# Optimization experiments

Measured on AMD Instinct MI355X. Metric: run time of the kernel, lower is better.

The kernel has to match this reference:

```python
import jax, jax.numpy as jnp
import numpy as np

B, N, HID, NHEADS, VOCAB = 8, 2048, 768, 4, 15
ALPHA = 0.2  # LeakyReLU negative slope
NEG = -9e15  # matches -9000000000000000.0 mask constant


def setup_inputs() -> dict:
    key = jax.random.key(0)
    ks = jax.random.split(key, 7)
    node_feats = jax.random.randint(ks[0], (B, N), 0, VOCAB, dtype=jnp.int32)
    adjs = jax.random.randint(ks[1], (B, N, N), 0, 2, dtype=jnp.int32)
    embed_table = jax.random.normal(ks[2], (VOCAB, HID), dtype=jnp.float32)
    W_heads = jax.random.normal(ks[3], (NHEADS, HID, HID), dtype=jnp.float32) * 0.05
    a_heads = jax.random.normal(ks[4], (NHEADS, 2 * HID, 1), dtype=jnp.float32) * 0.05
    W_out = jax.random.normal(ks[5], (NHEADS * HID, HID), dtype=jnp.float32) * 0.05
    a_out = jax.random.normal(ks[6], (2 * HID, 1), dtype=jnp.float32) * 0.05
    return {"node_feats": node_feats, "adjs": adjs, "embed_table": embed_table,
            "W_heads": W_heads, "a_heads": a_heads, "W_out": W_out, "a_out": a_out}


def gat_layer(h, adj, W, a, concat):
    # h: (B,N,Fin), adj: (B,N,N), W: (Fin,Fout), a: (2*Fout,1)
    Fout = W.shape[1]
    Wh = jnp.matmul(h, W)                      # (B,N,Fout)
    Wh1 = jnp.matmul(Wh, a[:Fout])             # (B,N,1)
    Wh2 = jnp.matmul(Wh, a[Fout:])             # (B,N,1)
    e = Wh1 + jnp.swapaxes(Wh2, 1, 2)          # (B,N,N)
    e = jax.nn.leaky_relu(e, negative_slope=ALPHA)
    e = jnp.where(adj > 0, e, NEG)
    att = jax.nn.softmax(e, axis=-1)           # (B,N,N)
    h_prime = jnp.matmul(att, Wh)              # (B,N,Fout)
    return jax.nn.elu(h_prime) if concat else h_prime


def reference(node_feats, adjs, embed_table, W_heads, a_heads, W_out, a_out):
    x = embed_table[node_feats]                # (B,N,HID)  (shape_enc treated as identity)
    # multi-head GAT, heads vmapped then concatenated along feature dim
    heads = jax.vmap(lambda W, a: gat_layer(x, adjs, W, a, concat=True))(W_heads, a_heads)
    x = jnp.concatenate(jnp.moveaxis(heads, 0, -2).reshape(B, N, 1, NHEADS * HID).squeeze(2)[None], axis=0)[0] if False else jnp.transpose(heads, (1, 2, 0, 3)).reshape(B, N, NHEADS * HID)
    x = jax.nn.elu(gat_layer(x, adjs, W_out, a_out, concat=False))  # (B,N,HID)
    # pooling_forward with all-ones mask -> masked mean over node dim
    sum_emb = jnp.sum(x, axis=1)               # (B,HID)
    denom = jnp.maximum(jnp.full_like(sum_emb, float(N)), 1e-9)
    return sum_emb / denom                     # (B,HID)
```

## Files before the change

kernel.cpp:

```cpp
#include <hip/hip_runtime.h>
#include <math.h>

#define BB 8
#define NN 2048
#define HID 768
#define NHEADS 4
#define VOCAB 15
#define ALPHA 0.2f
#define NEGV -9e15f
#define MTOT (BB * NN)

using short4v = __attribute__((ext_vector_type(4))) short;
using short8v = __attribute__((ext_vector_type(8))) short;
using f32x4 = __attribute__((ext_vector_type(4))) float;

__device__ __forceinline__ short f2bf(float f) {
  union { float f; unsigned u; } x;
  x.f = f;
  unsigned r = x.u + 0x7fffu + ((x.u >> 16) & 1u);
  return (short)(r >> 16);
}

__device__ __forceinline__ void cp16(const void* g, void* l) {
  __builtin_amdgcn_global_load_lds(
      (const __attribute__((address_space(1))) unsigned int*)g,
      (__attribute__((address_space(3))) unsigned int*)l, 16, 0, 0);
}

__device__ __forceinline__ unsigned long long nibcompress(unsigned long long x) {
  x = (x | (x >> 4)) & 0x00FF00FF00FF00FFull;
  x = (x | (x >> 8)) & 0x0000FFFF0000FFFFull;
  x = (x | (x >> 16)) & 0x00000000FFFFFFFFull;
  return x;
}

#define MEMFENCE asm volatile("" ::: "memory")
#define SBAR()                         \
  do {                                 \
    MEMFENCE;                          \
    __builtin_amdgcn_s_barrier();      \
    MEMFENCE;                          \
  } while (0)

#define PACK_B 32768
#define ZERO_B 308
#define NFM_B 64
#define TRAN_B 2304
#define TW_B 192
__global__ __launch_bounds__(256) void setup_kernel(
    const int* __restrict__ adj, unsigned long long* __restrict__ packed,
    float* __restrict__ zbase, const int* __restrict__ nf,
    unsigned long long* __restrict__ nfm, const float* __restrict__ W_out,
    short* __restrict__ Wt_o, const float* __restrict__ table,
    const float* __restrict__ W_heads, float* __restrict__ TWp) {
  const int bid = blockIdx.x;
  const int tid = threadIdx.x;
  if (bid < PACK_B) {
    __shared__ unsigned long long nibq[32];
    long base = (long)bid * 1024;
    int4 a = *(const int4*)(adj + base + tid * 4);
    unsigned nib = (a.x > 0 ? 1u : 0u) | (a.y > 0 ? 2u : 0u) |
                   (a.z > 0 ? 4u : 0u) | (a.w > 0 ? 8u : 0u);
    ((unsigned char*)nibq)[tid] = (unsigned char)nib;
    __syncthreads();
    if (tid < 16) {
      unsigned long long lo = nibcompress(nibq[2 * tid]);
      unsigned long long hi = nibcompress(nibq[2 * tid + 1]);
      packed[(base >> 6) + tid] = lo | (hi << 32);
    }
  } else if (bid < PACK_B + ZERO_B) {
    zbase[(bid - PACK_B) * 256 + tid] = 0.f;
  } else if (bid < PACK_B + ZERO_B + NFM_B) {
    int r = bid - PACK_B - ZERO_B;
    int b = r >> 3, c = r & 7;
    int w = tid >> 6;
    int j = c * 256 + tid;
    int nfv = nf[b * NN + j];
#pragma unroll
    for (int v = 0; v < VOCAB; ++v) {
      unsigned long long m = __ballot(nfv == v);
      if ((tid & 63) == 0) nfm[((long)b * VOCAB + v) * 32 + c * 4 + w] = m;
    }
  } else if (bid < PACK_B + ZERO_B + NFM_B + TRAN_B) {
    __shared__ float t[32][33];
    int r2 = bid - PACK_B - ZERO_B - NFM_B;
    const int K = NHEADS * HID, N = HID;
    int k0 = (r2 % 96) * 32, n0 = (r2 / 96) * 32;
    int tx = tid & 31, ty = tid >> 5;
#pragma unroll
    for (int i = 0; i < 32; i += 8)
      t[ty + i][tx] = W_out[(long)(k0 + ty + i) * N + n0 + tx];
    __syncthreads();
#pragma unroll
    for (int i = 0; i < 32; i += 8)
      Wt_o[(long)(n0 + ty + i) * K + k0 + tx] = f2bf(t[tx][ty + i]);
  } else {
    __shared__ float tbl[VOCAB][48];
    int r3 = bid - PACK_B - ZERO_B - NFM_B - TRAN_B;
    const int cx = r3 % 12, ky = r3 / 12;
    const int c = cx * 256 + tid;
    const int h = (cx * 256) / HID;
    const int n = c - h * HID;
    const int k0 = ky * 48;
    for (int idx = tid; idx < VOCAB * 48; idx += 256)
      tbl[idx / 48][idx % 48] = table[(idx / 48) * HID + k0 + idx % 48];
    __syncthreads();
    float acc[VOCAB];
#pragma unroll
    for (int v = 0; v < VOCAB; ++v) acc[v] = 0.f;
    const float* wp = W_heads + (long)h * HID * HID + (long)k0 * HID + n;
#pragma unroll 8
    for (int kk = 0; kk < 48; ++kk) {
      float w = wp[(long)kk * HID];
#pragma unroll
      for (int v = 0; v < VOCAB; ++v) acc[v] = fmaf(tbl[v][kk], w, acc[v]);
    }
#pragma unroll
    for (int v = 0; v < VOCAB; ++v)
      TWp[((long)ky * VOCAB + v) * (NHEADS * HID) + c] = acc[v];
  }
}

__global__ __launch_bounds__(256) void tw_finish_kernel(
    const float* __restrict__ TWp, float* __restrict__ TW,
    const float* __restrict__ a_heads, float* __restrict__ TW1,
    float* __restrict__ TW2) {
  const int tid = threadIdx.x;
  const int c = blockIdx.x * 256 + tid;
  const int h = (blockIdx.x * 256) / HID;
  const int n = c - h * HID;
  const float a1 = a_heads[h * 2 * HID + n];
  const float a2 = a_heads[h * 2 * HID + HID + n];
  const int lane = tid & 63;
  const int wv = tid >> 6;
  __shared__ float red[4][2 * VOCAB];

  float s1[VOCAB], s2[VOCAB];
#pragma unroll
  for (int v = 0; v < VOCAB; ++v) {
    float s = 0.f;
#pragma unroll
    for (int ky = 0; ky < 16; ++ky)
      s += TWp[((long)ky * VOCAB + v) * (NHEADS * HID) + c];
    TW[v * (NHEADS * HID) + c] = s;
    s1[v] = s * a1;
    s2[v] = s * a2;
  }
#pragma unroll
  for (int off = 1; off < 64; off <<= 1)
#pragma unroll
    for (int v = 0; v < VOCAB; ++v) {
      s1[v] += __shfl_xor(s1[v], off);
      s2[v] += __shfl_xor(s2[v], off);
    }
  if (lane == 0) {
#pragma unroll
    for (int v = 0; v < VOCAB; ++v) {
      red[wv][v] = s1[v];
      red[wv][VOCAB + v] = s2[v];
    }
  }
  __syncthreads();
  if (tid < 2 * VOCAB) {
    float s = red[0][tid] + red[1][tid] + red[2][tid] + red[3][tid];
    float* dst = (tid < VOCAB) ? (TW1 + h * VOCAB + tid)
                               : (TW2 + h * VOCAB + tid - VOCAB);
    atomicAdd(dst, s);
  }
}

__global__ __launch_bounds__(256) void p16_kernel(
    const int* __restrict__ nf, const unsigned* __restrict__ padj32,
    const unsigned* __restrict__ nfm32, const float* __restrict__ TW1,
    const float* __restrict__ TW2, float* __restrict__ P16) {
  const int t = threadIdx.x;
  const int wv = t >> 6;
  const int lane = t & 63;
  const int rowm = blockIdx.x * 4 + wv;
  const int b = rowm >> 11;
  __shared__ float cnts[4][16];

  unsigned a = padj32[(long)rowm * 64 + lane];
  const unsigned* nb = nfm32 + (long)b * VOCAB * 64 + lane;
  int cnt[VOCAB];
#pragma unroll
  for (int v = 0; v < VOCAB; ++v) cnt[v] = __popc(a & nb[v * 64]);
#pragma unroll
  for (int off = 1; off < 64; off <<= 1)
#pragma unroll
    for (int v = 0; v < VOCAB; ++v) cnt[v] += __shfl_xor(cnt[v], off);
  int cntsum = 0;
#pragma unroll
  for (int v = 0; v < VOCAB; ++v) cntsum += cnt[v];
  const bool use_full = (cntsum == 0);
  if (use_full) {
#pragma unroll
    for (int v = 0; v < VOCAB; ++v) cnt[v] = __popc(nb[v * 64]);
#pragma unroll
    for (int off = 1; off < 64; off <<= 1)
#pragma unroll
      for (int v = 0; v < VOCAB; ++v) cnt[v] += __shfl_xor(cnt[v], off);
  }
  if (lane < 16) cnts[wv][lane] = (lane < VOCAB) ? (float)cnt[lane] : 0.f;
  __syncthreads();

  const int h = lane >> 4;
  const int v = lane & 15;
  const int nfi = nf[b * NN + (rowm & 2047)];
  float cvf = cnts[wv][v];
  bool valid = (v < VOCAB) && (cvf > 0.f);
  float logit = 0.f;
  if (!use_full) {
    float s = TW1[h * VOCAB + nfi] + ((v < VOCAB) ? TW2[h * VOCAB + v] : 0.f);
    logit = s > 0.f ? s : ALPHA * s;
  }
  float mv = valid ? logit : -INFINITY;
#pragma unroll
  for (int off = 1; off < 16; off <<= 1) mv = fmaxf(mv, __shfl_xor(mv, off));
  float pv = valid ? cvf * __expf(logit - mv) : 0.f;
  float sum = pv;
#pragma unroll
  for (int off = 1; off < 16; off <<= 1) sum += __shfl_xor(sum, off);
  if (v < VOCAB) P16[((long)h * 16384 + rowm) * 16 + v] = pv / sum;
}

__global__ __launch_bounds__(256) void hcat_expand(
    const float* __restrict__ TW, const float* __restrict__ P16,
    short* __restrict__ hcat) {
  __shared__ float twl[VOCAB * 128];
  __shared__ float pl[128 * 16];
  const int c0 = blockIdx.x * 128;
  const int r0 = blockIdx.y * 128;
  const int h = c0 / HID;
  const int t = threadIdx.x;
  for (int idx = t; idx < VOCAB * 128; idx += 256)
    twl[idx] = TW[(idx / 128) * (NHEADS * HID) + c0 + (idx & 127)];
  for (int idx = t; idx < 128 * 16; idx += 256)
    pl[idx] = P16[((long)h * 16384 + r0 + (idx >> 4)) * 16 + (idx & 15)];
  __syncthreads();
  const int clb = (t & 31) * 4;
  const int rlb = (t >> 5) * 16;
#pragma unroll 4
  for (int rr = 0; rr < 16; ++rr) {
    int rl = rlb + rr;
    short4v o;
#pragma unroll
    for (int cc = 0; cc < 4; ++cc) {
      float s = 0.f;
#pragma unroll
      for (int vv = 0; vv < VOCAB; ++vv)
        s = fmaf(pl[rl * 16 + vv], twl[vv * 128 + clb + cc], s);
      s = s > 0.f ? s : (__expf(s) - 1.f);
      o[cc] = f2bf(s);
    }
    *(short4v*)(hcat + (long)(r0 + rl) * (NHEADS * HID) + c0 + clb) = o;
  }
}

template <int MODE>
__global__ __launch_bounds__(512, 2) void mfma_gemm(
    const short* __restrict__ A, const short* __restrict__ B,
    int K, int lda, int ldb, long sA, long sB,
    float* __restrict__ Cf, short* __restrict__ Ct,
    const float* __restrict__ a_vec, float* __restrict__ Wh1g,
    float* __restrict__ Wh2g) {
  __shared__ short lds[2][2][16384];

  const int gx = gridDim.x, gy = gridDim.y;
  int linb = blockIdx.x + gx * (blockIdx.y + gy * blockIdx.z);
  const int per = (gx * gy * gridDim.z) >> 3;
  int work = (linb & 7) * per + (linb >> 3);
  const int bx = work % gx;
  int tmpw = work / gx;
  const int by = tmpw % gy;
  const int z = tmpw / gy;

  A += (long)z * sA;
  B += (long)z * sB;

  const int tid = threadIdx.x;
  const int m0 = by * 256;
  const int n0 = bx * 256;
  const int lane = tid & 63;
  const int wid = tid >> 6;
  const int wr = wid >> 2;
  const int wc = wid & 3;
  const int l15 = lane & 15;
  const int quad = lane >> 4;
  const int NT = K >> 6;

  const int cbase = (quad ^ (l15 & 7)) << 3;

  auto stageA = [&](int kt, int h) {
    const short* src = A + (long)(m0 + h * 128) * lda + kt * 64;
    short* dst = &lds[kt & 1][0][h * 8192];
#pragma unroll
    for (int it = 0; it < 2; ++it) {
      int r = it * 64 + (tid >> 3);
      int s = tid & 7;
      cp16(src + (long)r * lda + ((s ^ (r & 7)) << 3),
           dst + (it * 512 + tid) * 8);
    }
  };
  auto stageB = [&](int kt, int h) {
    const short* src = B + (long)(n0 + h * 128) * ldb + kt * 64;
    short* dst = &lds[kt & 1][1][h * 8192];
#pragma unroll
    for (int it = 0; it < 2; ++it) {
      int r = it * 64 + (tid >> 3);
      int s = tid & 7;
      cp16(src + (long)r * ldb + ((s ^ (r & 7)) << 3),
           dst + (it * 512 + tid) * 8);
    }
  };

  f32x4 acc[8][4];
#pragma unroll
  for (int i = 0; i < 8; ++i)
#pragma unroll
    for (int j = 0; j < 4; ++j) acc[i][j] = (f32x4){0.f, 0.f, 0.f, 0.f};

  stageA(0, 0); stageA(0, 1);
  stageB(0, 0); stageB(0, 1);
  stageA(1, 0); stageA(1, 1);
  asm volatile("s_waitcnt vmcnt(4)" ::: "memory");
  SBAR();

#pragma unroll 1
  for (int t = 0; t < NT; ++t) {
    const int p = t & 1;
    const short* Ab = &lds[p][0][0];
    const short* Bb = &lds[p][1][0];
    short8v a[4][2], b0[2][2], b1[2][2];

    if (t + 1 < NT) { stageB(t + 1, 0); stageB(t + 1, 1); }
#pragma unroll
    for (int ii = 0; ii < 4; ++ii) {
      int ro = (wr * 128 + ii * 16 + l15) * 64;
      a[ii][0] = *(const short8v*)(Ab + ro + cbase);
      a[ii][1] = *(const short8v*)(Ab + ro + (cbase ^ 32));
    }
#pragma unroll
    for (int jj = 0; jj < 2; ++jj) {
      int ro = (wc * 64 + jj * 16 + l15) * 64;
      b0[jj][0] = *(const short8v*)(Bb + ro + cbase);
      b0[jj][1] = *(const short8v*)(Bb + ro + (cbase ^ 32));
    }
    SBAR();
    asm volatile("s_waitcnt lgkmcnt(0)" ::: "memory");
    __builtin_amdgcn_sched_barrier(0);
    __builtin_amdgcn_s_setprio(1);
#pragma unroll
    for (int ii = 0; ii < 4; ++ii)
#pragma unroll
      for (int jj = 0; jj < 2; ++jj) {
        acc[ii][jj] = __builtin_amdgcn_mfma_f32_16x16x32_bf16(
            a[ii][0], b0[jj][0], acc[ii][jj], 0, 0, 0);
        acc[ii][jj] = __builtin_amdgcn_mfma_f32_16x16x32_bf16(
            a[ii][1], b0[jj][1], acc[ii][jj], 0, 0, 0);
      }
    __builtin_amdgcn_sched_barrier(0);
    __builtin_amdgcn_s_setprio(0);
    SBAR();

#pragma unroll
    for (int jj = 0; jj < 2; ++jj) {
      int ro = (wc * 64 + 32 + jj * 16 + l15) * 64;
      b1[jj][0] = *(const short8v*)(Bb + ro + cbase);
      b1[jj][1] = *(const short8v*)(Bb + ro + (cbase ^ 32));
    }
    SBAR();
    asm volatile("s_waitcnt lgkmcnt(0)" ::: "memory");
    __builtin_amdgcn_sched_barrier(0);
    __builtin_amdgcn_s_setprio(1);
#pragma unroll
    for (int ii = 0; ii < 4; ++ii)
#pragma unroll
      for (int jj = 0; jj < 2; ++jj) {
        acc[ii][2 + jj] = __builtin_amdgcn_mfma_f32_16x16x32_bf16(
            a[ii][0], b1[jj][0], acc[ii][2 + jj], 0, 0, 0);
        acc[ii][2 + jj] = __builtin_amdgcn_mfma_f32_16x16x32_bf16(
            a[ii][1], b1[jj][1], acc[ii][2 + jj], 0, 0, 0);
      }
    __builtin_amdgcn_sched_barrier(0);
    __builtin_amdgcn_s_setprio(0);
    SBAR();

#pragma unroll
    for (int ii = 0; ii < 4; ++ii) {
      int ro = (wr * 128 + 64 + ii * 16 + l15) * 64;
      a[ii][0] = *(const short8v*)(Ab + ro + cbase);
      a[ii][1] = *(const short8v*)(Ab + ro + (cbase ^ 32));
    }
    SBAR();
    asm volatile("s_waitcnt lgkmcnt(0)" ::: "memory");
    __builtin_amdgcn_sched_barrier(0);
    __builtin_amdgcn_s_setprio(1);
#pragma unroll
    for (int ii = 0; ii < 4; ++ii)
#pragma unroll
      for (int jj = 0; jj < 2; ++jj) {
        acc[4 + ii][2 + jj] = __builtin_amdgcn_mfma_f32_16x16x32_bf16(
            a[ii][0], b1[jj][0], acc[4 + ii][2 + jj], 0, 0, 0);
        acc[4 + ii][2 + jj] = __builtin_amdgcn_mfma_f32_16x16x32_bf16(
            a[ii][1], b1[jj][1], acc[4 + ii][2 + jj], 0, 0, 0);
      }
    __builtin_amdgcn_sched_barrier(0);
    __builtin_amdgcn_s_setprio(0);
    SBAR();

    if (t + 2 < NT) { stageA(t + 2, 0); stageA(t + 2, 1); }
    __builtin_amdgcn_s_setprio(1);
#pragma unroll
    for (int ii = 0; ii < 4; ++ii)
#pragma unroll
      for (int jj = 0; jj < 2; ++jj) {
        acc[4 + ii][jj] = __builtin_amdgcn_mfma_f32_16x16x32_bf16(
            a[ii][0], b0[jj][0], acc[4 + ii][jj], 0, 0, 0);
        acc[4 + ii][jj] = __builtin_amdgcn_mfma_f32_16x16x32_bf16(
            a[ii][1], b0[jj][1], acc[4 + ii][jj], 0, 0, 0);
      }
    __builtin_amdgcn_sched_barrier(0);
    __builtin_amdgcn_s_setprio(0);
    if (t + 2 < NT) {
      asm volatile("s_waitcnt vmcnt(4)" ::: "memory");
    } else if (t + 1 < NT) {
      asm volatile("s_waitcnt vmcnt(0)" ::: "memory");
    }
    SBAR();
  }

  if constexpr (MODE == 3) {
#pragma unroll
    for (int nj = 0; nj < 4; ++nj) {
      int col = n0 + wc * 64 + nj * 16 + l15;
      float s = 0.f;
#pragma unroll
      for (int mi = 0; mi < 8; ++mi)
#pragma unroll
        for (int reg = 0; reg < 4; ++reg) {
          float v = acc[mi][nj][reg];
          s += v > 0.f ? v : (__expf(v) - 1.f);
        }
      s += __shfl_xor(s, 16);
      s += __shfl_xor(s, 32);
      if (quad == 0) atomicAdd(Cf + (long)z * HID + col, s * (1.0f / NN));
    }
  } else {
    float a1v[4], a2v[4];
#pragma unroll
    for (int nj = 0; nj < 4; ++nj) {
      int colh = n0 + wc * 64 + nj * 16 + l15;
      a1v[nj] = a_vec[colh];
      a2v[nj] = a_vec[HID + colh];
    }
#pragma unroll
    for (int mi = 0; mi < 8; ++mi) {
      int rb = m0 + wr * 128 + mi * 16 + quad * 4;
#pragma unroll
      for (int reg = 0; reg < 4; ++reg) {
        float s1 = 0.f, s2 = 0.f;
#pragma unroll
        for (int nj = 0; nj < 4; ++nj) {
          s1 = fmaf(acc[mi][nj][reg], a1v[nj], s1);
          s2 = fmaf(acc[mi][nj][reg], a2v[nj], s2);
        }
#pragma unroll
        for (int off = 1; off < 16; off <<= 1) {
          s1 += __shfl_xor(s1, off);
          s2 += __shfl_xor(s2, off);
        }
        if (l15 == 0) {
          atomicAdd(Wh1g + rb + reg, s1);
          atomicAdd(Wh2g + rb + reg, s2);
        }
      }
    }
    const int bb = m0 >> 11;
    const int ml0 = (m0 & 2047) + wr * 128;
#pragma unroll
    for (int mi = 0; mi < 8; ++mi) {
#pragma unroll
      for (int nj = 0; nj < 4; ++nj) {
        int colh = n0 + wc * 64 + nj * 16 + l15;
        short4v pk;
#pragma unroll
        for (int reg = 0; reg < 4; ++reg) pk[reg] = f2bf(acc[mi][nj][reg]);
        *(short4v*)(Ct + ((long)bb * HID + colh) * NN + ml0 + mi * 16 +
                    quad * 4) = pk;
      }
    }
  }
}

__global__ __launch_bounds__(256) void attn_softmax_kernel(
    const float* __restrict__ Wh1, const float* __restrict__ Wh2,
    const unsigned long long* __restrict__ packed, short* __restrict__ att,
    float* __restrict__ zA, int zn) {
  int row = blockIdx.x;
  if (row < zn) zA[row * 256 + threadIdx.x] = 0.f;
  int b = row >> 11;
  const unsigned char* bits = (const unsigned char*)(packed + (long)row * 32);
  const float* wh2b = Wh2 + b * NN;
  const int t = threadIdx.x;
  const int lane = t & 63;
  const int wv = t >> 6;

  unsigned m8 = bits[t];
  float wh1 = Wh1[row];
  float4 wa = ((const float4*)(wh2b + t * 8))[0];
  float4 wb = ((const float4*)(wh2b + t * 8))[1];
  float v[8] = {wa.x, wa.y, wa.z, wa.w, wb.x, wb.y, wb.z, wb.w};

  float lmax = -INFINITY;
#pragma unroll
  for (int k = 0; k < 8; ++k) {
    float s = wh1 + v[k];
    s = s > 0.f ? s : ALPHA * s;
    s = ((m8 >> k) & 1u) ? s : NEGV;
    v[k] = s;
    lmax = fmaxf(lmax, s);
  }

  __shared__ float redm[4], reds[4];
#pragma unroll
  for (int off = 32; off > 0; off >>= 1) lmax = fmaxf(lmax, __shfl_xor(lmax, off));
  if (lane == 0) redm[wv] = lmax;
  __syncthreads();
  float m = fmaxf(fmaxf(redm[0], redm[1]), fmaxf(redm[2], redm[3]));

  float lsum = 0.f;
#pragma unroll
  for (int k = 0; k < 8; ++k) {
    float p = __expf(v[k] - m);
    v[k] = p;
    lsum += p;
  }
#pragma unroll
  for (int off = 32; off > 0; off >>= 1) lsum += __shfl_xor(lsum, off);
  if (lane == 0) reds[wv] = lsum;
  __syncthreads();
  float inv = 1.f / (reds[0] + reds[1] + reds[2] + reds[3]);

  short8v o;
#pragma unroll
  for (int k = 0; k < 8; ++k) o[k] = f2bf(v[k] * inv);
  *(short8v*)(att + (long)row * NN + t * 8) = o;
}

extern "C" void kernel_launch(void* const* d_in, const int* in_sizes, int n_in,
                              void* d_out, int out_size, void* d_ws,
                              size_t ws_size, hipStream_t stream) {
  const int* node_feats = (const int*)d_in[0];
  const int* adjs = (const int*)d_in[1];
  const float* embed_table = (const float*)d_in[2];
  const float* W_heads = (const float*)d_in[3];
  const float* a_heads = (const float*)d_in[4];
  const float* W_out = (const float*)d_in[5];
  const float* a_out = (const float*)d_in[6];
  float* out = (float*)d_out;

  char* p = (char*)d_ws;
  short* Wt_o = (short*)p;  p += (size_t)HID * (NHEADS * HID) * 2;
  short* Wh_t = (short*)p;  p += (size_t)BB * HID * NN * 2;
  short* att2 = (short*)p;  p += (size_t)BB * NN * NN * 2;
  short* hcat = (short*)p;  p += (size_t)MTOT * NHEADS * HID * 2;
  unsigned long long* padj = (unsigned long long*)p;
  p += (size_t)BB * NN * NN / 8;
  float* P16 = (float*)p;   p += (size_t)NHEADS * 16384 * 16 * 4;
  float* Wh1 = (float*)p;   p += (size_t)16384 * 4;
  float* Wh2 = (float*)p;   p += (size_t)16384 * 4;
  float* TW1 = (float*)p;   p += (size_t)64 * 4;
  float* TW2 = (float*)p;   p += (size_t)64 * 4;
  p += (size_t)(ZERO_B * 256 - 2 * 16384 - 128) * 4;
  float* TWp = (float*)p;   p += (size_t)16 * VOCAB * NHEADS * HID * 4;
  float* TW = (float*)p;    p += (size_t)VOCAB * NHEADS * HID * 4;
  unsigned long long* nfm = (unsigned long long*)p;
  p += (size_t)BB * VOCAB * 32 * 8;
  if ((size_t)(p - (char*)d_ws) > ws_size) return;

  setup_kernel<<<PACK_B + ZERO_B + NFM_B + TRAN_B + TW_B, 256, 0, stream>>>(
      adjs, padj, Wh1, node_feats, nfm, W_out, Wt_o, embed_table, W_heads,
      TWp);

  tw_finish_kernel<<<12, 256, 0, stream>>>(TWp, TW, a_heads, TW1, TW2);
  p16_kernel<<<16384 / 4, 256, 0, stream>>>(
      node_feats, (const unsigned*)padj, (const unsigned*)nfm, TW1, TW2, P16);
  hcat_expand<<<dim3(24, 128), 256, 0, stream>>>(TW, P16, hcat);

  mfma_gemm<0><<<dim3(HID / 256, MTOT / 256, 1), 512, 0, stream>>>(
      hcat, Wt_o, NHEADS * HID, NHEADS * HID, NHEADS * HID, 0, 0,
      nullptr, Wh_t, a_out, Wh1, Wh2);
  attn_softmax_kernel<<<MTOT, 256, 0, stream>>>(Wh1, Wh2, padj, att2, out, 24);
  mfma_gemm<3><<<dim3(HID / 256, NN / 256, BB), 512, 0, stream>>>(
      att2, Wh_t, NN, NN, NN, (long)NN * NN, (long)HID * NN,
      out, nullptr, nullptr, nullptr, nullptr);
}
```

Baseline: 439.8 us.

## Generate GEMM A-operands on the fly instead of materializing hcat and attention matrices

Removes the hcat_expand kernel and the materialized bf16 attention matrix. In the first GEMM the A tile (ELU of P16·TW) is produced inside the kernel with small split-precision bf16 MFMAs, using hi/lo bf16 pairs to keep accuracy. In the second GEMM the unnormalized exp scores are built from Wh1/Wh2, the packed adjacency and the per-row max, and the row normalization is applied in the epilogue. The softmax kernel now emits only row stats. This cuts large global writes and reads (the B*N*N attention and the B*N*4*HID hcat) in exchange for extra in-kernel ALU/exp work and a single-buffered A tile that adds serialization.

```diff
diff --git a/kernel.cpp b/kernel.cpp
--- a/kernel.cpp
+++ b/kernel.cpp
@@ -19,6 +19,12 @@
   x.f = f;
   unsigned r = x.u + 0x7fffu + ((x.u >> 16) & 1u);
   return (short)(r >> 16);
+}
+
+__device__ __forceinline__ float b2f(short h) {
+  union { unsigned u; float f; } y;
+  y.u = ((unsigned)(unsigned short)h) << 16;
+  return y.f;
 }
 
 __device__ __forceinline__ void cp16(const void* g, void* l) {
@@ -122,7 +128,7 @@
 }
 
 __global__ __launch_bounds__(256) void tw_finish_kernel(
-    const float* __restrict__ TWp, float* __restrict__ TW,
+    const float* __restrict__ TWp, short* __restrict__ TWb,
     const float* __restrict__ a_heads, float* __restrict__ TW1,
     float* __restrict__ TW2) {
   const int tid = threadIdx.x;
@@ -135,6 +141,7 @@
   const int wv = tid >> 6;
   __shared__ float red[4][2 * VOCAB];
 
+  short* tb = TWb + ((long)c << 6);
   float s1[VOCAB], s2[VOCAB];
 #pragma unroll
   for (int v = 0; v < VOCAB; ++v) {
@@ -142,10 +149,16 @@
 #pragma unroll
     for (int ky = 0; ky < 16; ++ky)
       s += TWp[((long)ky * VOCAB + v) * (NHEADS * HID) + c];
-    TW[v * (NHEADS * HID) + c] = s;
+    short hi = f2bf(s);
+    short lo = f2bf(s - b2f(hi));
+    tb[v] = hi;
+    tb[16 + v] = hi;
+    tb[32 + v] = lo;
+    tb[48 + v] = lo;
     s1[v] = s * a1;
     s2[v] = s * a2;
   }
+  tb[15] = 0; tb[31] = 0; tb[47] = 0; tb[63] = 0;
 #pragma unroll
   for (int off = 1; off < 64; off <<= 1)
 #pragma unroll
@@ -172,7 +185,7 @@
 __global__ __launch_bounds__(256) void p16_kernel(
     const int* __restrict__ nf, const unsigned* __restrict__ padj32,
     const unsigned* __restrict__ nfm32, const float* __restrict__ TW1,
-    const float* __restrict__ TW2, float* __restrict__ P16) {
+    const float* __restrict__ TW2, short* __restrict__ P2) {
   const int t = threadIdx.x;
   const int wv = t >> 6;
   const int lane = t & 63;
@@ -221,62 +234,46 @@
   float sum = pv;
 #pragma unroll
   for (int off = 1; off < 16; off <<= 1) sum += __shfl_xor(sum, off);
-  if (v < VOCAB) P16[((long)h * 16384 + rowm) * 16 + v] = pv / sum;
-}
-
-__global__ __launch_bounds__(256) void hcat_expand(
-    const float* __restrict__ TW, const float* __restrict__ P16,
-    short* __restrict__ hcat) {
-  __shared__ float twl[VOCAB * 128];
-  __shared__ float pl[128 * 16];
-  const int c0 = blockIdx.x * 128;
-  const int r0 = blockIdx.y * 128;
-  const int h = c0 / HID;
-  const int t = threadIdx.x;
-  for (int idx = t; idx < VOCAB * 128; idx += 256)
-    twl[idx] = TW[(idx / 128) * (NHEADS * HID) + c0 + (idx & 127)];
-  for (int idx = t; idx < 128 * 16; idx += 256)
-    pl[idx] = P16[((long)h * 16384 + r0 + (idx >> 4)) * 16 + (idx & 15)];
-  __syncthreads();
-  const int clb = (t & 31) * 4;
-  const int rlb = (t >> 5) * 16;
-#pragma unroll 4
-  for (int rr = 0; rr < 16; ++rr) {
-    int rl = rlb + rr;
-    short4v o;
-#pragma unroll
-    for (int cc = 0; cc < 4; ++cc) {
-      float s = 0.f;
-#pragma unroll
-      for (int vv = 0; vv < VOCAB; ++vv)
-        s = fmaf(pl[rl * 16 + vv], twl[vv * 128 + clb + cc], s);
-      s = s > 0.f ? s : (__expf(s) - 1.f);
-      o[cc] = f2bf(s);
-    }
-    *(short4v*)(hcat + (long)(r0 + rl) * (NHEADS * HID) + c0 + clb) = o;
-  }
+  float pn = pv / sum;
+  short hi = f2bf(pn);
+  short lo = f2bf(pn - b2f(hi));
+  long pb = ((long)h * 16384 + rowm) << 5;
+  P2[pb + v] = hi;
+  P2[pb + 16 + v] = lo;
 }
 
 template <int MODE>
 __global__ __launch_bounds__(512, 2) void mfma_gemm(
-    const short* __restrict__ A, const short* __restrict__ B,
-    int K, int lda, int ldb, long sA, long sB,
+    const short* __restrict__ Bm, int K, int ldb, long sB,
+    const short* __restrict__ P2, const short* __restrict__ TWb,
+    const float* __restrict__ Wh1r, const float* __restrict__ Wh2r,
+    const unsigned long long* __restrict__ packed,
+    const float* __restrict__ mrow, const float* __restrict__ invs,
     float* __restrict__ Cf, short* __restrict__ Ct,
     const float* __restrict__ a_vec, float* __restrict__ Wh1g,
     float* __restrict__ Wh2g) {
-  __shared__ short lds[2][2][16384];
+  __shared__ short Bs[2][16384];
+  __shared__ short At[16384];
+  __shared__ float whl[2048];
 
   const int gx = gridDim.x, gy = gridDim.y;
   int linb = blockIdx.x + gx * (blockIdx.y + gy * blockIdx.z);
   const int per = (gx * gy * gridDim.z) >> 3;
   int work = (linb & 7) * per + (linb >> 3);
-  const int bx = work % gx;
-  int tmpw = work / gx;
-  const int by = tmpw % gy;
-  const int z = tmpw / gy;
-
-  A += (long)z * sA;
-  B += (long)z * sB;
+  int bx, by, z;
+  if constexpr (MODE == 0) {
+    bx = work / gy;
+    by = work % gy;
+    z = 0;
+  } else {
+    bx = work % gx;
+    int tm = work / gx;
+    by = tm % gy;
+    z = tm / gy;
+  }
+
+  Bm += (long)z * sB;
+  const long zr0 = (long)z * NN;
 
   const int tid = threadIdx.x;
   const int m0 = by * 256;
@@ -288,23 +285,11 @@
   const int l15 = lane & 15;
   const int quad = lane >> 4;
   const int NT = K >> 6;
-
   const int cbase = (quad ^ (l15 & 7)) << 3;
 
-  auto stageA = [&](int kt, int h) {
-    const short* src = A + (long)(m0 + h * 128) * lda + kt * 64;
-    short* dst = &lds[kt & 1][0][h * 8192];
-#pragma unroll
-    for (int it = 0; it < 2; ++it) {
-      int r = it * 64 + (tid >> 3);
-      int s = tid & 7;
-      cp16(src + (long)r * lda + ((s ^ (r & 7)) << 3),
-           dst + (it * 512 + tid) * 8);
-    }
-  };
-  auto stageB = [&](int kt, int h) {
-    const short* src = B + (long)(n0 + h * 128) * ldb + kt * 64;
-    short* dst = &lds[kt & 1][1][h * 8192];
+  auto stageB_ = [&](int kt, int h) {
+    const short* src = Bm + (long)(n0 + h * 128) * ldb + kt * 64;
+    short* dst = &Bs[kt & 1][h * 8192];
 #pragma unroll
     for (int it = 0; it < 2; ++it) {
       int r = it * 64 + (tid >> 3);
@@ -314,26 +299,97 @@
     }
   };
 
+  short8v gA0, gA1, gBh[4], gBl[4];
+  const short* pbT = nullptr;
+  unsigned mk = 0;
+  float wh1v = 0.f, mrv = 0.f;
+  const int gr = tid >> 1, gkh = tid & 1;
+
+  auto genA_mfma = [&]() {
+#pragma unroll
+    for (int f = 0; f < 2; ++f) {
+      short8v Af = f ? gA1 : gA0;
+#pragma unroll
+      for (int cg = 0; cg < 4; ++cg) {
+        f32x4 e = __builtin_amdgcn_mfma_f32_16x16x32_bf16(
+            Af, gBh[cg], (f32x4){0.f, 0.f, 0.f, 0.f}, 0, 0, 0);
+        e = __builtin_amdgcn_mfma_f32_16x16x32_bf16(Af, gBl[cg], e, 0, 0, 0);
+#pragma unroll
+        for (int reg = 0; reg < 4; ++reg) {
+          float v = e[reg];
+          v = v > 0.f ? v : (__expf(v) - 1.f);
+          int row = wid * 32 + f * 16 + quad * 4 + reg;
+          int c = cg * 16 + l15;
+          At[row * 64 + (((c >> 3) ^ (row & 7)) << 3) + (c & 7)] = f2bf(v);
+        }
+      }
+    }
+  };
+
+  auto genA_exp = [&](int kt1) {
+    const float4* wp = (const float4*)(whl + kt1 * 64 + gkh * 32);
+    float wv[32];
+#pragma unroll
+    for (int cc = 0; cc < 8; ++cc) {
+      float4 q = wp[cc];
+      wv[cc * 4 + 0] = q.x; wv[cc * 4 + 1] = q.y;
+      wv[cc * 4 + 2] = q.z; wv[cc * 4 + 3] = q.w;
+    }
+#pragma unroll
+    for (int c = 0; c < 4; ++c) {
+      short8v o;
+#pragma unroll
+      for (int e = 0; e < 8; ++e) {
+        int j = c * 8 + e;
+        float s = wh1v + wv[j];
+        float l = fmaxf(s, ALPHA * s);
+        float ex = __expf(l - mrv);
+        o[e] = ((mk >> j) & 1u) ? f2bf(ex) : (short)0;
+      }
+      *(short8v*)(At + gr * 64 + ((((gkh << 2) + c) ^ (gr & 7)) << 3)) = o;
+    }
+  };
+
   f32x4 acc[8][4];
 #pragma unroll
   for (int i = 0; i < 8; ++i)
 #pragma unroll
     for (int j = 0; j < 4; ++j) acc[i][j] = (f32x4){0.f, 0.f, 0.f, 0.f};
 
-  stageA(0, 0); stageA(0, 1);
-  stageB(0, 0); stageB(0, 1);
-  stageA(1, 0); stageA(1, 1);
-  asm volatile("s_waitcnt vmcnt(4)" ::: "memory");
+  stageB_(0, 0);
+  stageB_(0, 1);
+  if constexpr (MODE == 0) {
+    const short* pa = P2 + (((long)(m0 + wid * 32 + l15)) << 5) + quad * 8;
+    gA0 = *(const short8v*)pa;
+    gA1 = *(const short8v*)(pa + 512);
+    pbT = TWb + (((long)l15) << 6) + quad * 8;
+#pragma unroll
+    for (int cg = 0; cg < 4; ++cg) {
+      gBh[cg] = *(const short8v*)(pbT + (cg << 10));
+      gBl[cg] = *(const short8v*)(pbT + (cg << 10) + 32);
+    }
+  } else {
+    ((float4*)whl)[tid] = ((const float4*)(Wh2r + zr0))[tid];
+    wh1v = Wh1r[zr0 + m0 + gr];
+    mrv = mrow[zr0 + m0 + gr];
+    mk = *(const unsigned*)((const char*)packed +
+                            ((long)(zr0 + m0 + gr)) * 256 + gkh * 4);
+  }
+  asm volatile("s_waitcnt vmcnt(0)" ::: "memory");
+  asm volatile("s_waitcnt lgkmcnt(0)" ::: "memory");
+  SBAR();
+  if constexpr (MODE == 0) genA_mfma(); else genA_exp(0);
+  asm volatile("s_waitcnt lgkmcnt(0)" ::: "memory");
   SBAR();
 
 #pragma unroll 1
   for (int t = 0; t < NT; ++t) {
     const int p = t & 1;
-    const short* Ab = &lds[p][0][0];
-    const short* Bb = &lds[p][1][0];
+    const short* Ab = At;
+    const short* Bb = Bs[p];
     short8v a[4][2], b0[2][2], b1[2][2];
 
-    if (t + 1 < NT) { stageB(t + 1, 0); stageB(t + 1, 1); }
+    if (t + 1 < NT) { stageB_(t + 1, 0); stageB_(t + 1, 1); }
 #pragma unroll
     for (int ii = 0; ii < 4; ++ii) {
       int ro = (wr * 128 + ii * 16 + l15) * 64;
@@ -386,6 +442,20 @@
     __builtin_amdgcn_s_setprio(0);
     SBAR();
 
+    if (t + 1 < NT) {
+      if constexpr (MODE == 0) {
+        int kt1 = t + 1, h1 = kt1 / 12;
+        const short* pa =
+            P2 + (((long)h1 * 16384 + m0 + wid * 32 + l15) << 5) + quad * 8;
+        gA0 = *(const short8v*)pa;
+        gA1 = *(const short8v*)(pa + 512);
+        pbT = TWb + (((long)(kt1 * 64 + l15)) << 6) + quad * 8;
+      } else {
+        mk = *(const unsigned*)((const char*)packed +
+                                ((long)(zr0 + m0 + gr)) * 256 + (t + 1) * 8 +
+                                gkh * 4);
+      }
+    }
 #pragma unroll
     for (int ii = 0; ii < 4; ++ii) {
       int ro = (wr * 128 + 64 + ii * 16 + l15) * 64;
@@ -409,7 +479,15 @@
     __builtin_amdgcn_s_setprio(0);
     SBAR();
 
-    if (t + 2 < NT) { stageA(t + 2, 0); stageA(t + 2, 1); }
+    if (t + 1 < NT) {
+      if constexpr (MODE == 0) {
+#pragma unroll
+        for (int cg = 0; cg < 4; ++cg) {
+          gBh[cg] = *(const short8v*)(pbT + (cg << 10));
+          gBl[cg] = *(const short8v*)(pbT + (cg << 10) + 32);
+        }
+      }
+    }
     __builtin_amdgcn_s_setprio(1);
 #pragma unroll
     for (int ii = 0; ii < 4; ++ii)
@@ -422,15 +500,22 @@
       }
     __builtin_amdgcn_sched_barrier(0);
     __builtin_amdgcn_s_setprio(0);
-    if (t + 2 < NT) {
-      asm volatile("s_waitcnt vmcnt(4)" ::: "memory");
-    } else if (t + 1 < NT) {
+    if (t + 1 < NT) {
       asm volatile("s_waitcnt vmcnt(0)" ::: "memory");
+      if constexpr (MODE == 0) genA_mfma(); else genA_exp(t + 1);
+      asm volatile("s_waitcnt lgkmcnt(0)" ::: "memory");
     }
     SBAR();
   }
 
   if constexpr (MODE == 3) {
+    float ivv[8][4];
+#pragma unroll
+    for (int mi = 0; mi < 8; ++mi)
+#pragma unroll
+      for (int reg = 0; reg < 4; ++reg)
+        ivv[mi][reg] =
+            invs[zr0 + m0 + wr * 128 + mi * 16 + quad * 4 + reg];
 #pragma unroll
     for (int nj = 0; nj < 4; ++nj) {
       int col = n0 + wc * 64 + nj * 16 + l15;
@@ -439,7 +524,7 @@
       for (int mi = 0; mi < 8; ++mi)
 #pragma unroll
         for (int reg = 0; reg < 4; ++reg) {
-          float v = acc[mi][nj][reg];
+          float v = acc[mi][nj][reg] * ivv[mi][reg];
           s += v > 0.f ? v : (__expf(v) - 1.f);
         }
       s += __shfl_xor(s, 16);
@@ -493,10 +578,10 @@
   }
 }
 
-__global__ __launch_bounds__(256) void attn_softmax_kernel(
+__global__ __launch_bounds__(256) void attn_stats_kernel(
     const float* __restrict__ Wh1, const float* __restrict__ Wh2,
-    const unsigned long long* __restrict__ packed, short* __restrict__ att,
-    float* __restrict__ zA, int zn) {
+    const unsigned long long* __restrict__ packed, float* __restrict__ mr,
+    float* __restrict__ iv, float* __restrict__ zA, int zn) {
   int row = blockIdx.x;
   if (row < zn) zA[row * 256 + threadIdx.x] = 0.f;
   int b = row >> 11;
@@ -531,21 +616,15 @@
 
   float lsum = 0.f;
 #pragma unroll
-  for (int k = 0; k < 8; ++k) {
-    float p = __expf(v[k] - m);
-    v[k] = p;
-    lsum += p;
-  }
+  for (int k = 0; k < 8; ++k) lsum += __expf(v[k] - m);
 #pragma unroll
   for (int off = 32; off > 0; off >>= 1) lsum += __shfl_xor(lsum, off);
   if (lane == 0) reds[wv] = lsum;
   __syncthreads();
-  float inv = 1.f / (reds[0] + reds[1] + reds[2] + reds[3]);
-
-  short8v o;
-#pragma unroll
-  for (int k = 0; k < 8; ++k) o[k] = f2bf(v[k] * inv);
-  *(short8v*)(att + (long)row * NN + t * 8) = o;
+  if (t == 0) {
+    mr[row] = m;
+    iv[row] = 1.f / (reds[0] + reds[1] + reds[2] + reds[3]);
+  }
 }
 
 extern "C" void kernel_launch(void* const* d_in, const int* in_sizes, int n_in,
@@ -563,18 +642,18 @@
   char* p = (char*)d_ws;
   short* Wt_o = (short*)p;  p += (size_t)HID * (NHEADS * HID) * 2;
   short* Wh_t = (short*)p;  p += (size_t)BB * HID * NN * 2;
-  short* att2 = (short*)p;  p += (size_t)BB * NN * NN * 2;
-  short* hcat = (short*)p;  p += (size_t)MTOT * NHEADS * HID * 2;
+  short* P2 = (short*)p;    p += (size_t)NHEADS * 16384 * 32 * 2;
+  short* TWb = (short*)p;   p += (size_t)(NHEADS * HID) * 64 * 2;
   unsigned long long* padj = (unsigned long long*)p;
   p += (size_t)BB * NN * NN / 8;
-  float* P16 = (float*)p;   p += (size_t)NHEADS * 16384 * 16 * 4;
   float* Wh1 = (float*)p;   p += (size_t)16384 * 4;
   float* Wh2 = (float*)p;   p += (size_t)16384 * 4;
   float* TW1 = (float*)p;   p += (size_t)64 * 4;
   float* TW2 = (float*)p;   p += (size_t)64 * 4;
-  p += (size_t)(ZERO_B * 256 - 2 * 16384 - 128) * 4;
+  float* mrow = (float*)p;  p += (size_t)16384 * 4;
+  float* invs = (float*)p;  p += (size_t)16384 * 4;
+  p += (size_t)(ZERO_B * 256 - 4 * 16384 - 128) * 4;
   float* TWp = (float*)p;   p += (size_t)16 * VOCAB * NHEADS * HID * 4;
-  float* TW = (float*)p;    p += (size_t)VOCAB * NHEADS * HID * 4;
   unsigned long long* nfm = (unsigned long long*)p;
   p += (size_t)BB * VOCAB * 32 * 8;
   if ((size_t)(p - (char*)d_ws) > ws_size) return;
@@ -583,16 +662,16 @@
       adjs, padj, Wh1, node_feats, nfm, W_out, Wt_o, embed_table, W_heads,
       TWp);
 
-  tw_finish_kernel<<<12, 256, 0, stream>>>(TWp, TW, a_heads, TW1, TW2);
+  tw_finish_kernel<<<12, 256, 0, stream>>>(TWp, TWb, a_heads, TW1, TW2);
   p16_kernel<<<16384 / 4, 256, 0, stream>>>(
-      node_feats, (const unsigned*)padj, (const unsigned*)nfm, TW1, TW2, P16);
-  hcat_expand<<<dim3(24, 128), 256, 0, stream>>>(TW, P16, hcat);
+      node_feats, (const unsigned*)padj, (const unsigned*)nfm, TW1, TW2, P2);
 
   mfma_gemm<0><<<dim3(HID / 256, MTOT / 256, 1), 512, 0, stream>>>(
-      hcat, Wt_o, NHEADS * HID, NHEADS * HID, NHEADS * HID, 0, 0,
-      nullptr, Wh_t, a_out, Wh1, Wh2);
-  attn_softmax_kernel<<<MTOT, 256, 0, stream>>>(Wh1, Wh2, padj, att2, out, 24);
+      Wt_o, NHEADS * HID, NHEADS * HID, 0, P2, TWb, nullptr, nullptr, nullptr,
+      nullptr, nullptr, nullptr, Wh_t, a_out, Wh1, Wh2);
+  attn_stats_kernel<<<MTOT, 256, 0, stream>>>(Wh1, Wh2, padj, mrow, invs, out,
+                                              24);
   mfma_gemm<3><<<dim3(HID / 256, NN / 256, BB), 512, 0, stream>>>(
-      att2, Wh_t, NN, NN, NN, (long)NN * NN, (long)HID * NN,
-      out, nullptr, nullptr, nullptr, nullptr);
-}
+      Wh_t, NN, NN, (long)HID * NN, nullptr, nullptr, Wh1, Wh2, padj, mrow,
+      invs, out, nullptr, nullptr, nullptr, nullptr);
+}
```

Result: slower. 662.6 us (+50.7%).
